# Performance work log

Measured on AMD Instinct MI355X. Metric: run time of the kernel, lower is better.

## Reference

```python
import jax, jax.numpy as jnp
import numpy as np

HID, HEADS = 2048, 16
HD = HID // HEADS  # head_dim = 128
EPS = 1e-6


def rope_tables(head_dim, max_pos, base=10000.0):
    inv = 1.0 / (base ** (jnp.arange(0, head_dim, 2, dtype=jnp.float32) / head_dim))
    t = jnp.arange(max_pos, dtype=jnp.float32)
    freqs = jnp.outer(t, inv)                      # [max_pos, d/2]
    emb = jnp.concatenate([freqs, freqs], axis=-1)  # [max_pos, d]
    return jnp.cos(emb), jnp.sin(emb)


def rotate_half(x):
    x1, x2 = jnp.split(x, 2, axis=-1)
    return jnp.concatenate([-x2, x1], axis=-1)


def lf_gate(x, c1w, c1b, c2w, c2b, rms_w):
    # x: [b, s, h]; prompt phase -> lf1/lf2 caches are zeros -> zero-pad 1 step on time axis
    xt = jnp.transpose(x, (0, 2, 1))[..., None]                 # [b, h, s, 1]
    xt = jnp.pad(xt, ((0, 0), (0, 0), (1, 0), (0, 0)))           # [b, h, s+1, 1]
    dn = ('NCHW', 'OIHW', 'NCHW')
    o1 = jax.lax.conv_general_dilated(xt, c1w, (1, 1), 'VALID', dimension_numbers=dn)
    o1 = o1 + c1b[None, :, None, None]                           # [b, h/2, s, 1]
    o1 = jnp.pad(o1, ((0, 0), (0, 0), (1, 0), (0, 0)))           # [b, h/2, s+1, 1]
    o2 = jax.lax.conv_general_dilated(o1, c2w, (1, 1), 'VALID', dimension_numbers=dn)
    o2 = o2 + c2b[None, :, None, None]                           # [b, h, s, 1]
    y = jnp.transpose(o2[..., 0], (0, 2, 1)) + x                 # residual, [b, s, h]
    var = jnp.mean(y * y, axis=-1, keepdims=True)
    return y * jax.lax.rsqrt(var + EPS) * rms_w


def setup_inputs() -> dict:
    key = jax.random.key(0)
    ks = jax.random.split(key, 10)
    b, s = 2, 2048
    inp = {
        'hidden_states': jax.random.normal(ks[0], (b, s, HID), jnp.float32),
        'positions': jnp.arange(s, dtype=jnp.int32),
        'wq': jax.random.normal(ks[1], (HID, HID), jnp.float32) * 0.02,
        'wk': jax.random.normal(ks[2], (HID, HID), jnp.float32) * 0.02,
        'wv': jax.random.normal(ks[3], (HID, HID), jnp.float32) * 0.02,
        'wo': jax.random.normal(ks[4], (HID, HID), jnp.float32) * 0.02,
        'conv1_w': jax.random.normal(ks[5], (HID // 2, HID, 2, 1), jnp.float32) * 0.02,
        'conv1_b': jnp.zeros((HID // 2,), jnp.float32),
        'conv2_w': jax.random.normal(ks[6], (HID, HID // 2, 2, 1), jnp.float32) * 0.02,
        'conv2_b': jnp.zeros((HID,), jnp.float32),
        'rms_w': jnp.ones((HID,), jnp.float32),
    }
    return inp


def reference(hidden_states, positions, wq, wk, wv, wo, conv1_w, conv1_b, conv2_w, conv2_b, rms_w):
    b, s, _ = hidden_states.shape
    # value projection from raw hidden states (pre-gate)
    v = (hidden_states @ wv).reshape(b, s, HEADS, HD)            # [b, s, H, d]
    # localized-filtering gate (prompt phase: zero caches)
    h = lf_gate(hidden_states, conv1_w, conv1_b, conv2_w, conv2_b, rms_w)
    q = h @ wq                                                   # [b, s, H*d]
    k = h @ wk
    # faithful Yuan quirk: concat q,k then reshape to [b,s,H,2d] and chunk
    qk = jnp.concatenate([q, k], axis=-1).reshape(b, s, HEADS, 2 * HD)
    q, k = jnp.split(qk, 2, axis=-1)                             # each [b, s, H, d]
    # rotary
    cos, sin = rope_tables(HD, 8192)
    c = cos[positions][None, :, None, :]                         # [1, s, 1, d]
    sn = sin[positions][None, :, None, :]
    q = q * c + rotate_half(q) * sn
    k = k * c + rotate_half(k) * sn
    # causal attention (paged attention reduces to this for the prompt)
    scale = HD ** -0.5
    scores = jnp.einsum('bqhd,bkhd->bhqk', q, k) * scale         # [b, H, s, s]
    mask = jnp.tril(jnp.ones((s, s), dtype=bool))
    scores = jnp.where(mask[None, None], scores, jnp.finfo(scores.dtype).min)
    probs = jax.nn.softmax(scores, axis=-1)
    out = jnp.einsum('bhqk,bkhd->bqhd', probs, v).reshape(b, s, HEADS * HD)
    return out @ wo
```

## Files before the change

### kernel.cpp

```cpp
#include <hip/hip_runtime.h>

#define HID 2048
#define HEADS 16
#define HD 128
#define BATCH 2
#define S 2048
#define ROWS (BATCH*S)

typedef short short8 __attribute__((ext_vector_type(8)));
typedef unsigned short ushort4v __attribute__((ext_vector_type(4)));
typedef unsigned short ushort2v __attribute__((ext_vector_type(2)));
typedef float f32x4 __attribute__((ext_vector_type(4)));
typedef __bf16 bf16x8 __attribute__((ext_vector_type(8)));
typedef __bf16 bf16x4 __attribute__((ext_vector_type(4)));

static __device__ __forceinline__ float b2f(unsigned short u) {
  union { float f; unsigned int i; } v; v.i = ((unsigned int)u) << 16; return v.f;
}
static __device__ __forceinline__ unsigned short f2b(float f) {
  union { float f; unsigned int i; } v; v.f = f;
  unsigned int u = v.i;
  unsigned int r = ((u >> 16) & 1u) + 0x7fffu;
  return (unsigned short)((u + r) >> 16);
}

static __device__ __forceinline__ void gload_lds16(const unsigned short* g, unsigned short* l) {
  __builtin_amdgcn_global_load_lds(
      (const __attribute__((address_space(1))) unsigned int*)(const void*)g,
      (__attribute__((address_space(3))) unsigned int*)(void*)l,
      16, 0, 0);
}

__global__ void fill_debug(unsigned short* __restrict__ out, long n) {
  long i = (long)blockIdx.x * blockDim.x + threadIdx.x;
  if (i < n) out[i] = 0x447A;
}

__global__ void prep_all(const float* __restrict__ c1w, const float* __restrict__ c2w,
                         const float* __restrict__ x, const int* __restrict__ positions,
                         const float* __restrict__ c1b, const float* __restrict__ c2b,
                         const float* __restrict__ rmsw,
                         unsigned short* __restrict__ w1t0, unsigned short* __restrict__ w1t1,
                         unsigned short* __restrict__ w2t0, unsigned short* __restrict__ w2t1,
                         unsigned short* __restrict__ xb,
                         float* __restrict__ ctab, float* __restrict__ stab,
                         unsigned short* __restrict__ c1bb, unsigned short* __restrict__ c2bb,
                         unsigned short* __restrict__ rmswb, unsigned short* __restrict__ zpg) {
  int job = blockIdx.y;
  if (job == 0 || job == 1) {
    const float* w = (job == 0) ? c1w : c2w;
    unsigned short* o0 = (job == 0) ? w1t0 : w2t0;
    unsigned short* o1 = (job == 0) ? w1t1 : w2t1;
    long i = (long)blockIdx.x * 256 + threadIdx.x;
    f32x4 v = *(const f32x4*)(w + i*4);
    ushort2v a = { f2b(v[0]), f2b(v[2]) };
    ushort2v b = { f2b(v[1]), f2b(v[3]) };
    *(ushort2v*)(o0 + i*2) = a;
    *(ushort2v*)(o1 + i*2) = b;
  } else if (job == 2) {
    long i = (long)blockIdx.x * 256 + threadIdx.x;
    #pragma unroll
    for (int rep = 0; rep < 2; ++rep) {
      long idx = i + (long)rep * 1048576L;
      f32x4 v = *(const f32x4*)(x + idx*4);
      ushort4v o = { f2b(v[0]), f2b(v[1]), f2b(v[2]), f2b(v[3]) };
      *(ushort4v*)(xb + idx*4) = o;
    }
  } else {
    int bx = blockIdx.x;
    if (bx < 512) {
      int t = bx * 4 + (threadIdx.x >> 6);
      int i = threadIdx.x & 63;
      float pos = (float)positions[t];
      float inv = powf(10000.0f, -(float)i / 64.0f);
      float ang = pos * inv;
      float sv, cv;
      sincosf(ang, &sv, &cv);
      ctab[t*64 + i] = cv;
      stab[t*64 + i] = sv;
    } else if (bx < 544) {
      int i = (bx - 512) * 256 + threadIdx.x;
      if (i < 1024) c1bb[i] = f2b(c1b[i]);
      if (i < 2048) { c2bb[i] = f2b(c2b[i]); rmswb[i] = f2b(rmsw[i]); }
      zpg[i] = 0;
    }
  }
}

__global__ void transpose4(const float* __restrict__ s0, const float* __restrict__ s1,
                           const float* __restrict__ s2, const float* __restrict__ s3,
                           unsigned short* __restrict__ d0, unsigned short* __restrict__ d1,
                           unsigned short* __restrict__ d2, unsigned short* __restrict__ d3) {
  __shared__ unsigned short tl[64][73];
  const float* in; unsigned short* out; int perm;
  switch (blockIdx.z) {
    case 0:  in = s0; out = d0; perm = 1; break;
    case 1:  in = s1; out = d1; perm = 1; break;
    case 2:  in = s2; out = d2; perm = 0; break;
    default: in = s3; out = d3; perm = 0; break;
  }
  int n0 = blockIdx.x * 64, k0 = blockIdx.y * 64;
  int tid = threadIdx.x;
  int r = tid >> 3, c8 = (tid & 7) * 8;
  #pragma unroll
  for (int j = 0; j < 2; ++j) {
    int rr = r + j*32;
    const float* p = in + (size_t)(k0 + rr)*HID + n0 + c8;
    f32x4 v0 = *(const f32x4*)p;
    f32x4 v1 = *(const f32x4*)(p + 4);
    #pragma unroll
    for (int e = 0; e < 4; ++e) { tl[rr][c8 + e] = f2b(v0[e]); tl[rr][c8 + 4 + e] = f2b(v1[e]); }
  }
  __syncthreads();
  #pragma unroll
  for (int j = 0; j < 2; ++j) {
    int rr = r + j*32;
    int orow = n0 + rr;
    if (perm) {
      int s5 = (orow >> 5) & 3;
      s5 = (s5 == 1) ? 2 : (s5 == 2) ? 1 : s5;
      orow = (orow & ~127) | (s5 << 5) | (orow & 31);
    }
    short8 v;
    #pragma unroll
    for (int e = 0; e < 8; ++e) v[e] = (short)tl[c8 + e][rr];
    *(short8*)(out + (size_t)orow*HID + k0 + c8) = v;
  }
}


struct SPtrs { const unsigned short* p[6]; };

static __device__ __forceinline__ void build_ptrs(SPtrs& sp,
    const unsigned short* Ap, const unsigned short* Bp, int Ksz, int sh,
    int m0, int n0, const unsigned short* zpg, int tid) {
  int lane = tid & 63;
  int scol = (((lane & 7) * 16) ^ (((lane >> 3) & 7) << 4)) >> 1;
  #pragma unroll
  for (int j = 0; j < 2; ++j) {
    int row = ((tid >> 6) * 2 + j) * 8 + (lane >> 3);
    int gr = m0 + row;
    sp.p[j]     = (sh && ((gr & (S - 1)) == 0)) ? (zpg + scol)
                                                : (Ap + (size_t)(gr - sh)*Ksz + scol);
    sp.p[2 + j] = Bp + (size_t)(n0 + row)*Ksz + scol;
    sp.p[4 + j] = Bp + (size_t)(n0 + 128 + row)*Ksz + scol;
  }
}

static __device__ __forceinline__ void stage6(unsigned short* buf, SPtrs& sp, int tid) {
  int c0 = (tid >> 6) * 1024;
  gload_lds16(sp.p[0], buf + c0);
  gload_lds16(sp.p[1], buf + c0 + 512);
  gload_lds16(sp.p[2], buf + 8192  + c0);
  gload_lds16(sp.p[3], buf + 8192  + c0 + 512);
  gload_lds16(sp.p[4], buf + 16384 + c0);
  gload_lds16(sp.p[5], buf + 16384 + c0 + 512);
  #pragma unroll
  for (int i = 0; i < 6; ++i) sp.p[i] += 64;
}

static __device__ __forceinline__ void rd_af(const unsigned short* Ah, bf16x8 (&afr)[4][2],
                                             int wm, int lr, int col0, int axor) {
  #pragma unroll
  for (int mi = 0; mi < 4; ++mi) {
    const unsigned short* rp = Ah + (wm*64 + mi*16 + lr) * 64;
    #pragma unroll
    for (int kk = 0; kk < 2; ++kk)
      afr[mi][kk] = *(const bf16x8*)(rp + (((kk*64 + col0) ^ axor) >> 1));
  }
}
static __device__ __forceinline__ void rd_bf(const unsigned short* Bh, bf16x8 (&bfr)[2][2],
                                             int wn, int lr, int col0, int axor) {
  #pragma unroll
  for (int ni = 0; ni < 2; ++ni) {
    const unsigned short* rp = Bh + (wn*32 + ni*16 + lr) * 64;
    #pragma unroll
    for (int kk = 0; kk < 2; ++kk)
      bfr[ni][kk] = *(const bf16x8*)(rp + (((kk*64 + col0) ^ axor) >> 1));
  }
}
static __device__ __forceinline__ void mfma16(const bf16x8 (&afr)[4][2], const bf16x8 (&bfr)[2][2],
                                              f32x4 (&ac)[4][2]) {
  #pragma unroll
  for (int kk = 0; kk < 2; ++kk)
    #pragma unroll
    for (int mi = 0; mi < 4; ++mi)
      #pragma unroll
      for (int ni = 0; ni < 2; ++ni)
        ac[mi][ni] = __builtin_amdgcn_mfma_f32_16x16x32_bf16(afr[mi][kk], bfr[ni][kk], ac[mi][ni], 0, 0, 0);
}

static __device__ __forceinline__ void gemm8_core(
    unsigned short* lds,
    const unsigned short* __restrict__ A1, const unsigned short* __restrict__ A2,
    const unsigned short* __restrict__ B1, const unsigned short* __restrict__ B2,
    int K1, int K2,
    const unsigned short* __restrict__ bias, const unsigned short* __restrict__ resid,
    void* __restrict__ Cout, int outmode, int N, int m0, int n0,
    int a1shift, const unsigned short* __restrict__ zrow) {
  int tid = threadIdx.x;
  int lane = tid & 63, w = tid >> 6;
  int wm = w >> 2, wn = w & 3;
  int lr = lane & 15, g = lane >> 4;
  int col0 = g * 16;
  int axor = (lr & 7) << 4;
  int nk1 = K1 >> 6;
  int nk = (K1 + K2) >> 6;
  f32x4 acc[2][4][2] = {};
  bf16x8 afr[4][2], bfr0[2][2], bfr1[2][2];

  unsigned short* buf0 = lds;
  unsigned short* buf1 = lds + 24576;
  unsigned short* buf2 = lds + 49152;

  SPtrs sp;
  build_ptrs(sp, A1, B1, K1, a1shift, m0, n0, zrow, tid);

  stage6(buf0, sp, tid);
  stage6(buf1, sp, tid);

  unsigned short* cur = buf0;
  unsigned short* nx1 = buf1;
  unsigned short* nx2 = buf2;
  for (int t = 0; t < nk; ++t) {
    if (t < nk - 1) asm volatile("s_waitcnt vmcnt(6)" ::: "memory");
    else            asm volatile("s_waitcnt vmcnt(0)" ::: "memory");
    __builtin_amdgcn_s_barrier();
    asm volatile("" ::: "memory");

    rd_af(cur,         afr,  wm, lr, col0, axor);
    rd_bf(cur + 8192,  bfr0, wn, lr, col0, axor);
    rd_bf(cur + 16384, bfr1, wn, lr, col0, axor);
    if (t + 2 < nk) {
      if (t + 2 == nk1) build_ptrs(sp, A2, B2, K2, 0, m0, n0, zrow, tid);
      stage6(nx2, sp, tid);
    }
    __builtin_amdgcn_s_setprio(1);
    mfma16(afr, bfr0, acc[0]);
    mfma16(afr, bfr1, acc[1]);
    __builtin_amdgcn_s_setprio(0);

    unsigned short* tmp = cur; cur = nx1; nx1 = nx2; nx2 = tmp;
  }

  #pragma unroll
  for (int qn = 0; qn < 2; ++qn)
    #pragma unroll
    for (int mi = 0; mi < 4; ++mi) {
      int row0 = m0 + wm*64 + mi*16 + g*4;
      #pragma unroll
      for (int ni = 0; ni < 2; ++ni) {
        int col = n0 + qn*128 + wn*32 + ni*16 + lr;
        float bv = bias ? b2f(bias[col]) : 0.f;
        f32x4 a = acc[qn][mi][ni];
        if (outmode == 3) {
          int bb = row0 >> 11;
          int s0 = row0 & (S - 1);
          size_t base = ((size_t)bb * HID + col) * S + s0;
          ushort4v pk;
          #pragma unroll
          for (int j = 0; j < 4; ++j) pk[j] = f2b(a[j]);
          *(ushort4v*)((unsigned short*)Cout + base) = pk;
        } else {
          #pragma unroll
          for (int j = 0; j < 4; ++j) {
            size_t idx = (size_t)(row0 + j) * N + col;
            float v = a[j] + bv;
            if (resid) v += b2f(resid[idx]);
            if (outmode == 1) ((float*)Cout)[idx] = v;
            else ((unsigned short*)Cout)[idx] = f2b(v);
          }
        }
      }
    }
}

template<int SHIFT>
__launch_bounds__(512, 1)
__global__ void gemm8_bt(const unsigned short* __restrict__ A1,
                         const unsigned short* __restrict__ A2,
                         const unsigned short* __restrict__ B1,
                         const unsigned short* __restrict__ B2,
                         int K1, int K2,
                         const unsigned short* __restrict__ bias,
                         const unsigned short* __restrict__ resid,
                         void* __restrict__ Cout, int outmode, int N,
                         const unsigned short* __restrict__ zrow) {
  __shared__ __align__(16) unsigned short lds[73728];
  gemm8_core(lds, A1, A2, B1, B2, K1, K2, bias, resid, Cout, outmode, N,
             blockIdx.x*128, blockIdx.y*256, SHIFT, zrow);
}

struct GemmJob {
  const unsigned short *A1, *A2, *B1, *B2;
  int K1, K2;
  const unsigned short *bias;
  void* Cout; int outmode; int N; int nby; int a1shift;
};

__launch_bounds__(512, 1)
__global__ void gemm8_dual(GemmJob j0, GemmJob j1, const unsigned short* __restrict__ zrow) {
  __shared__ __align__(16) unsigned short lds[73728];
  int by = blockIdx.y;
  GemmJob j;
  if (by < j0.nby) { j = j0; } else { j = j1; by -= j0.nby; }
  gemm8_core(lds, j.A1, j.A2, j.B1, j.B2, j.K1, j.K2, j.bias, nullptr,
             j.Cout, j.outmode, j.N, blockIdx.x*128, by*256, j.a1shift, zrow);
}

__global__ void rmsnorm_rows(const unsigned short* __restrict__ y,
                             const unsigned short* __restrict__ w,
                             unsigned short* __restrict__ out) {
  int r = blockIdx.x;
  int c8 = threadIdx.x * 8;
  const unsigned short* yr = y + (size_t)r * HID;
  short8 v = *(const short8*)(yr + c8);
  float f[8];
  float ss = 0.f;
  #pragma unroll
  for (int e = 0; e < 8; ++e) { f[e] = b2f((unsigned short)v[e]); ss += f[e]*f[e]; }
  #pragma unroll
  for (int o = 32; o; o >>= 1) ss += __shfl_xor(ss, o);
  __shared__ float red[4];
  if ((threadIdx.x & 63) == 0) red[threadIdx.x >> 6] = ss;
  __syncthreads();
  float tot = red[0] + red[1] + red[2] + red[3];
  float scale = rsqrtf(tot / (float)HID + 1e-6f);
  short8 wv = *(const short8*)(w + c8);
  short8 o8;
  #pragma unroll
  for (int e = 0; e < 8; ++e) o8[e] = (short)f2b(f[e] * scale * b2f((unsigned short)wv[e]));
  *(short8*)(out + (size_t)r*HID + c8) = o8;
}

__global__ void rope_rearrange(const unsigned short* __restrict__ qkf,
                               const float* __restrict__ ctab, const float* __restrict__ stab,
                               unsigned short* __restrict__ qr, unsigned short* __restrict__ kr) {
  int r = blockIdx.x;
  int t = r & (S - 1);
  int h = threadIdx.x >> 4;
  int i4 = (threadIdx.x & 15) * 4;
  int pc = (i4 & 31) + ((i4 >> 5) << 6);
  const unsigned short* qk = qkf + (size_t)r * (2*HID) + h * 256;
  f32x4 c = *(const f32x4*)(ctab + t*64 + i4);
  f32x4 s = *(const f32x4*)(stab + t*64 + i4);
  ushort4v q1 = *(const ushort4v*)(qk + pc);
  ushort4v q2 = *(const ushort4v*)(qk + pc + 32);
  ushort4v k1 = *(const ushort4v*)(qk + 128 + pc);
  ushort4v k2 = *(const ushort4v*)(qk + 128 + pc + 32);
  size_t o = (size_t)r * HID + (size_t)h * HD;
  const float SC = 0.08838834764831845f * 1.44269504088896340f;
  ushort4v oq1, oq2, ok1, ok2;
  #pragma unroll
  for (int e = 0; e < 4; ++e) {
    float a = b2f(q1[e]), b = b2f(q2[e]);
    float x = b2f(k1[e]), y = b2f(k2[e]);
    oq1[e] = f2b((a*c[e] - b*s[e]) * SC);
    oq2[e] = f2b((b*c[e] + a*s[e]) * SC);
    ok1[e] = f2b(x*c[e] - y*s[e]);
    ok2[e] = f2b(y*c[e] + x*s[e]);
  }
  *(ushort4v*)(qr + o + i4)      = oq1;
  *(ushort4v*)(qr + o + 64 + i4) = oq2;
  *(ushort4v*)(kr + o + i4)      = ok1;
  *(ushort4v*)(kr + o + 64 + i4) = ok2;
}

#define KT 64

__launch_bounds__(256, 2)
__global__ void attn_mfma(const unsigned short* __restrict__ Qr,
                          const unsigned short* __restrict__ Kr,
                          const unsigned short* __restrict__ Vt,
                          unsigned short* __restrict__ Out) {
  __shared__ __align__(16) unsigned short lds[36864];
  int tid = threadIdx.x, lane = tid & 63, w = tid >> 6;
  int bh = blockIdx.x;
  int b = bh >> 4, h = bh & 15;
  int qt = (int)gridDim.y - 1 - (int)blockIdx.y;
  int q0 = qt * 64;
  size_t bS = (size_t)b * S;
  size_t ho = (size_t)h * HD;
  int lr = lane & 15, g = lane >> 4;
  int rsw = (lr & 7) << 3;
  bf16x8 bq[4];
  {
    int qrow = q0 + w*16 + lr;
    const unsigned short* qp = Qr + (bS + qrow)*HID + ho + g*8;
    #pragma unroll
    for (int kk = 0; kk < 4; ++kk) bq[kk] = *(const bf16x8*)(qp + kk*32);
  }
  const unsigned short* kp[4];
  const unsigned short* vp[4];
  #pragma unroll
  for (int j = 0; j < 4; ++j) {
    int c = w*4 + j;
    int rk = c*4 + (lane >> 4);
    int sck = ((lane & 15) * 8) ^ ((rk & 7) << 3);
    kp[j] = Kr + (bS + rk)*HID + ho + sck;
    int rv = c*8 + (lane >> 3);
    int scv = ((lane & 7) * 8) ^ ((rv & 7) << 3);
    vp[j] = Vt + ((size_t)b*HID + ho + rv)*S + scv;
  }
  int cdst = (w*4) * 512;
  unsigned short* curK = lds;
  unsigned short* curV = lds + 8192;
  unsigned short* nxtK = lds + 16384;
  unsigned short* nxtV = lds + 24576;
  #pragma unroll
  for (int j = 0; j < 4; ++j) {
    gload_lds16(kp[j], curK + cdst + j*512);
    gload_lds16(vp[j], curV + cdst + j*512);
    kp[j] += (size_t)KT * HID;
    vp[j] += KT;
  }
  f32x4 o[8] = {};
  float m = -1e30f, l = 0.f;
  unsigned short* PlW = lds + 32768 + w*1024;
  int ntiles = qt + 1;
  for (int kt = 0; kt < ntiles; ++kt) {
    asm volatile("s_waitcnt vmcnt(0)" ::: "memory");
    __builtin_amdgcn_s_barrier();
    asm volatile("" ::: "memory");
    if (kt + 1 < ntiles) {
      #pragma unroll
      for (int j = 0; j < 4; ++j) {
        gload_lds16(kp[j], nxtK + cdst + j*512);
        gload_lds16(vp[j], nxtV + cdst + j*512);
        kp[j] += (size_t)KT * HID;
        vp[j] += KT;
      }
    }
    f32x4 st[4] = {};
    __builtin_amdgcn_s_setprio(1);
    #pragma unroll
    for (int kk = 0; kk < 4; ++kk) {
      #pragma unroll
      for (int mi = 0; mi < 4; ++mi) {
        bf16x8 a = *(const bf16x8*)(&curK[(mi*16 + lr)*128 + ((kk*32 + g*8) ^ rsw)]);
        st[mi] = __builtin_amdgcn_mfma_f32_16x16x32_bf16(a, bq[kk], st[mi], 0, 0, 0);
      }
    }
    __builtin_amdgcn_s_setprio(0);
    bool lastt = (kt == ntiles - 1);
    float tm = -1e30f;
    #pragma unroll
    for (int mi = 0; mi < 4; ++mi)
      #pragma unroll
      for (int r = 0; r < 4; ++r) {
        float v = st[mi][r];
        if (lastt && (mi*16 + 4*g + r) > (w*16 + lr)) v = -1e30f;
        st[mi][r] = v;
        tm = fmaxf(tm, v);
      }
    tm = fmaxf(tm, __shfl_xor(tm, 16));
    tm = fmaxf(tm, __shfl_xor(tm, 32));
    if (!__all(tm - m <= 11.5f)) {
      float mn = fmaxf(m, tm);
      float sc = exp2f(m - mn);
      float s0 = __shfl(sc, 4*g+0), s1 = __shfl(sc, 4*g+1);
      float s2 = __shfl(sc, 4*g+2), s3 = __shfl(sc, 4*g+3);
      #pragma unroll
      for (int ni = 0; ni < 8; ++ni) {
        o[ni][0] *= s0; o[ni][1] *= s1; o[ni][2] *= s2; o[ni][3] *= s3;
      }
      l *= sc;
      m = mn;
    }
    float ts = 0.f;
    __bf16 pbf[4][4];
    #pragma unroll
    for (int mi = 0; mi < 4; ++mi)
      #pragma unroll
      for (int r = 0; r < 4; ++r) {
        float p = exp2f(st[mi][r] - m);
        ts += p;
        pbf[mi][r] = (__bf16)p;
      }
    ts += __shfl_xor(ts, 16);
    ts += __shfl_xor(ts, 32);
    l += ts;
    #pragma unroll
    for (int mi = 0; mi < 4; ++mi) {
      bf16x4 pk = { pbf[mi][0], pbf[mi][1], pbf[mi][2], pbf[mi][3] };
      *(bf16x4*)(&PlW[lr*64 + ((mi*16 + 4*g) ^ rsw)]) = pk;
    }
    asm volatile("" ::: "memory");
    __builtin_amdgcn_s_setprio(1);
    #pragma unroll
    for (int kk = 0; kk < 2; ++kk) {
      int pc = (kk*32 + g*8) ^ rsw;
      bf16x8 a = *(const bf16x8*)(&PlW[lr*64 + pc]);
      #pragma unroll
      for (int ni = 0; ni < 8; ++ni) {
        bf16x8 bv = *(const bf16x8*)(&curV[(ni*16 + lr)*64 + pc]);
        o[ni] = __builtin_amdgcn_mfma_f32_16x16x32_bf16(a, bv, o[ni], 0, 0, 0);
      }
    }
    __builtin_amdgcn_s_setprio(0);
    unsigned short* t0 = curK; curK = nxtK; nxtK = t0;
    unsigned short* t1 = curV; curV = nxtV; nxtV = t1;
  }
  float l0 = __shfl(l, 4*g+0), l1 = __shfl(l, 4*g+1);
  float l2 = __shfl(l, 4*g+2), l3 = __shfl(l, 4*g+3);
  float i0 = 1.f/l0, i1 = 1.f/l1, i2 = 1.f/l2, i3 = 1.f/l3;
  int rbase = q0 + w*16 + 4*g;
  #pragma unroll
  for (int ni = 0; ni < 8; ++ni) {
    size_t cbase = ho + ni*16 + lr;
    Out[(bS + rbase + 0)*HID + cbase] = f2b(o[ni][0]*i0);
    Out[(bS + rbase + 1)*HID + cbase] = f2b(o[ni][1]*i1);
    Out[(bS + rbase + 2)*HID + cbase] = f2b(o[ni][2]*i2);
    Out[(bS + rbase + 3)*HID + cbase] = f2b(o[ni][3]*i3);
  }
}

extern "C" void kernel_launch(void* const* d_in, const int* in_sizes, int n_in,
                              void* d_out, int out_size, void* d_ws, size_t ws_size,
                              hipStream_t stream) {
  const float* x_raw   = (const float*)d_in[0];
  const int* positions = (const int*)d_in[1];
  const float* wq_raw  = (const float*)d_in[2];
  const float* wk_raw  = (const float*)d_in[3];
  const float* wv_raw  = (const float*)d_in[4];
  const float* wo_raw  = (const float*)d_in[5];
  const float* c1w_raw = (const float*)d_in[6];
  const float* c1b_raw = (const float*)d_in[7];
  const float* c2w_raw = (const float*)d_in[8];
  const float* c2b_raw = (const float*)d_in[9];
  const float* rms_raw = (const float*)d_in[10];

  const size_t WS_NEEDED = 140000000;
  if (ws_size < WS_NEEDED) {
    long n = (long)out_size;
    fill_debug<<<dim3((unsigned)((n + 255) / 256)), dim3(256), 0, stream>>>((unsigned short*)d_out, n);
    return;
  }

  char* ws = (char*)d_ws;
  size_t off = 0;
  auto alloc = [&](size_t bytes) { char* p = ws + off; off += (bytes + 255) & ~(size_t)255; return p; };
  float* ctab          = (float*)alloc((size_t)S*64*4);
  float* stab          = (float*)alloc((size_t)S*64*4);
  unsigned short* wqkt = (unsigned short*)alloc((size_t)2*HID*HID*2);
  unsigned short* wvt  = (unsigned short*)alloc((size_t)HID*HID*2);
  unsigned short* wot  = (unsigned short*)alloc((size_t)HID*HID*2);
  unsigned short* w1t0 = (unsigned short*)alloc((size_t)1024*HID*2);
  unsigned short* w1t1 = (unsigned short*)alloc((size_t)1024*HID*2);
  unsigned short* w2t0 = (unsigned short*)alloc((size_t)HID*1024*2);
  unsigned short* w2t1 = (unsigned short*)alloc((size_t)HID*1024*2);
  unsigned short* xb   = (unsigned short*)alloc((size_t)ROWS*HID*2);
  unsigned short* qrb  = (unsigned short*)alloc((size_t)ROWS*HID*2);
  unsigned short* o1   = (unsigned short*)alloc((size_t)ROWS*1024*2);
  unsigned short* yb   = (unsigned short*)alloc((size_t)ROWS*HID*2);
  unsigned short* hg   = (unsigned short*)alloc((size_t)ROWS*HID*2);
  unsigned short* qkf  = (unsigned short*)alloc((size_t)ROWS*2*HID*2);
  unsigned short* vtg  = (unsigned short*)alloc((size_t)BATCH*HID*S*2);
  unsigned short* c1bb = (unsigned short*)alloc(1024*2);
  unsigned short* c2bb = (unsigned short*)alloc(2048*2);
  unsigned short* rmswb= (unsigned short*)alloc(2048*2);
  unsigned short* zpg  = (unsigned short*)alloc(8192*2);
  unsigned short* krr  = xb;
  unsigned short* attn = yb;

  dim3 b256(256);
  dim3 b512(512);
  prep_all<<<dim3(4096, 4), b256, 0, stream>>>(c1w_raw, c2w_raw, x_raw, positions,
                                               c1b_raw, c2b_raw, rms_raw,
                                               w1t0, w1t1, w2t0, w2t1, xb,
                                               ctab, stab, c1bb, c2bb, rmswb, zpg);
  transpose4<<<dim3(32,32,4), b256, 0, stream>>>(wq_raw, wk_raw, wv_raw, wo_raw,
                                                 wqkt, wqkt + (size_t)HID*HID, wvt, wot);
  {
    GemmJob j0 = { xb, xb, w1t0, w1t1, HID, HID, c1bb, o1, 0, 1024, 4, 1 };
    GemmJob j1 = { xb, xb, wvt,  wvt,  HID, 0,   nullptr, vtg, 3, HID, 8, 0 };
    gemm8_dual<<<dim3(ROWS/128, 12), b512, 0, stream>>>(j0, j1, zpg);
  }
  gemm8_bt<1><<<dim3(ROWS/128, HID/256), b512, 0, stream>>>(o1, o1, w2t0, w2t1, 1024, 1024, c2bb, xb, yb, 0, HID, zpg);
  rmsnorm_rows<<<dim3(ROWS), b256, 0, stream>>>(yb, rmswb, hg);
  gemm8_bt<0><<<dim3(ROWS/128, (2*HID)/256), b512, 0, stream>>>(hg, hg, wqkt, wqkt, HID, 0, nullptr, nullptr, qkf, 0, 2*HID, nullptr);
  rope_rearrange<<<dim3(ROWS), b256, 0, stream>>>(qkf, ctab, stab, qrb, krr);
  attn_mfma<<<dim3(BATCH*HEADS, S/64), b256, 0, stream>>>(qrb, krr, vtg, attn);
  gemm8_bt<0><<<dim3(ROWS/128, HID/256), b512, 0, stream>>>(attn, attn, wot, wot, HID, 0, nullptr, nullptr, d_out, 1, HID, nullptr);
}
```

Measured before the change: 368.2 us.

## Switch attention to 32x32x16 MFMA with 128-row query tiles and register P

The attention kernel now uses 32x32x16 bf16 MFMA instead of 16x16x32, with each wave owning 32 query rows, so a block covers 128 queries and the grid halves. The softmax probabilities stay in registers and are redistributed with cross-half shuffles instead of going through LDS, which removes the P staging buffer and its LDS traffic. Causal masking now applies only to tiles that cross the diagonal. This doubles reuse of each K/V tile loaded per block and cuts LDS reads, but it raises register pressure, halves the number of blocks, and computes some fully masked work near the diagonal for waves whose rows sit lower in the tile.

```diff
diff --git a/kernel.cpp b/kernel.cpp
--- a/kernel.cpp
+++ b/kernel.cpp
@@ -11,8 +11,10 @@
 typedef unsigned short ushort4v __attribute__((ext_vector_type(4)));
 typedef unsigned short ushort2v __attribute__((ext_vector_type(2)));
 typedef float f32x4 __attribute__((ext_vector_type(4)));
+typedef float f32x16 __attribute__((ext_vector_type(16)));
 typedef __bf16 bf16x8 __attribute__((ext_vector_type(8)));
 typedef __bf16 bf16x4 __attribute__((ext_vector_type(4)));
+typedef __bf16 bf16x2 __attribute__((ext_vector_type(2)));
 
 static __device__ __forceinline__ float b2f(unsigned short u) {
   union { float f; unsigned int i; } v; v.i = ((unsigned int)u) << 16; return v.f;
@@ -373,22 +375,21 @@
                           const unsigned short* __restrict__ Kr,
                           const unsigned short* __restrict__ Vt,
                           unsigned short* __restrict__ Out) {
-  __shared__ __align__(16) unsigned short lds[36864];
+  __shared__ __align__(16) unsigned short lds[32768];
   int tid = threadIdx.x, lane = tid & 63, w = tid >> 6;
   int bh = blockIdx.x;
   int b = bh >> 4, h = bh & 15;
   int qt = (int)gridDim.y - 1 - (int)blockIdx.y;
-  int q0 = qt * 64;
+  int q0w = qt * 128 + w * 32;
   size_t bS = (size_t)b * S;
   size_t ho = (size_t)h * HD;
-  int lr = lane & 15, g = lane >> 4;
-  int rsw = (lr & 7) << 3;
-  bf16x8 bq[4];
+  int l31 = lane & 31, hi = lane >> 5;
+  int rsw = (lane & 7) << 3;
+  bf16x8 bq[8];
   {
-    int qrow = q0 + w*16 + lr;
-    const unsigned short* qp = Qr + (bS + qrow)*HID + ho + g*8;
-    #pragma unroll
-    for (int kk = 0; kk < 4; ++kk) bq[kk] = *(const bf16x8*)(qp + kk*32);
+    const unsigned short* qp = Qr + (bS + q0w + l31)*HID + ho + hi*8;
+    #pragma unroll
+    for (int kk = 0; kk < 8; ++kk) bq[kk] = *(const bf16x8*)(qp + kk*16);
   }
   const unsigned short* kp[4];
   const unsigned short* vp[4];
@@ -414,10 +415,9 @@
     kp[j] += (size_t)KT * HID;
     vp[j] += KT;
   }
-  f32x4 o[8] = {};
+  f32x16 o2[4] = {};
   float m = -1e30f, l = 0.f;
-  unsigned short* PlW = lds + 32768 + w*1024;
-  int ntiles = qt + 1;
+  int ntiles = 2*qt + 2;
   for (int kt = 0; kt < ntiles; ++kt) {
     asm volatile("s_waitcnt vmcnt(0)" ::: "memory");
     __builtin_amdgcn_s_barrier();
@@ -431,87 +431,99 @@
         vp[j] += KT;
       }
     }
-    f32x4 st[4] = {};
+    f32x16 st0 = {}, st1 = {};
     __builtin_amdgcn_s_setprio(1);
     #pragma unroll
-    for (int kk = 0; kk < 4; ++kk) {
-      #pragma unroll
-      for (int mi = 0; mi < 4; ++mi) {
-        bf16x8 a = *(const bf16x8*)(&curK[(mi*16 + lr)*128 + ((kk*32 + g*8) ^ rsw)]);
-        st[mi] = __builtin_amdgcn_mfma_f32_16x16x32_bf16(a, bq[kk], st[mi], 0, 0, 0);
+    for (int kk = 0; kk < 8; ++kk) {
+      bf16x8 a0 = *(const bf16x8*)(&curK[(l31)*128      + ((kk*16 + hi*8) ^ rsw)]);
+      bf16x8 a1 = *(const bf16x8*)(&curK[(32 + l31)*128 + ((kk*16 + hi*8) ^ rsw)]);
+      st0 = __builtin_amdgcn_mfma_f32_32x32x16_bf16(a0, bq[kk], st0, 0, 0, 0);
+      st1 = __builtin_amdgcn_mfma_f32_32x32x16_bf16(a1, bq[kk], st1, 0, 0, 0);
+    }
+    __builtin_amdgcn_s_setprio(0);
+    int kbase = kt * 64;
+    float tm = -1e30f;
+    if (kbase + 63 > q0w) {
+      int qg = q0w + l31;
+      #pragma unroll
+      for (int r = 0; r < 16; ++r) {
+        int crow = (r&3) + 8*(r>>2) + 4*hi;
+        if (kbase + crow > qg)      st0[r] = -1e30f;
+        if (kbase + 32 + crow > qg) st1[r] = -1e30f;
+        tm = fmaxf(tm, fmaxf(st0[r], st1[r]));
       }
-    }
-    __builtin_amdgcn_s_setprio(0);
-    bool lastt = (kt == ntiles - 1);
-    float tm = -1e30f;
-    #pragma unroll
-    for (int mi = 0; mi < 4; ++mi)
-      #pragma unroll
-      for (int r = 0; r < 4; ++r) {
-        float v = st[mi][r];
-        if (lastt && (mi*16 + 4*g + r) > (w*16 + lr)) v = -1e30f;
-        st[mi][r] = v;
-        tm = fmaxf(tm, v);
-      }
-    tm = fmaxf(tm, __shfl_xor(tm, 16));
+    } else {
+      #pragma unroll
+      for (int r = 0; r < 16; ++r) tm = fmaxf(tm, fmaxf(st0[r], st1[r]));
+    }
     tm = fmaxf(tm, __shfl_xor(tm, 32));
     if (!__all(tm - m <= 11.5f)) {
       float mn = fmaxf(m, tm);
       float sc = exp2f(m - mn);
-      float s0 = __shfl(sc, 4*g+0), s1 = __shfl(sc, 4*g+1);
-      float s2 = __shfl(sc, 4*g+2), s3 = __shfl(sc, 4*g+3);
-      #pragma unroll
-      for (int ni = 0; ni < 8; ++ni) {
-        o[ni][0] *= s0; o[ni][1] *= s1; o[ni][2] *= s2; o[ni][3] *= s3;
+      #pragma unroll
+      for (int r = 0; r < 16; ++r) {
+        int crow = (r&3) + 8*(r>>2) + 4*hi;
+        float scv = __shfl(sc, crow);
+        #pragma unroll
+        for (int ni = 0; ni < 4; ++ni) o2[ni][r] *= scv;
       }
       l *= sc;
       m = mn;
     }
     float ts = 0.f;
-    __bf16 pbf[4][4];
-    #pragma unroll
-    for (int mi = 0; mi < 4; ++mi)
-      #pragma unroll
-      for (int r = 0; r < 4; ++r) {
-        float p = exp2f(st[mi][r] - m);
-        ts += p;
-        pbf[mi][r] = (__bf16)p;
-      }
-    ts += __shfl_xor(ts, 16);
+    unsigned int u0[8], u1[8];
+    #pragma unroll
+    for (int j = 0; j < 8; ++j) {
+      float a0 = exp2f(st0[2*j] - m), b0 = exp2f(st0[2*j+1] - m);
+      float a1 = exp2f(st1[2*j] - m), b1 = exp2f(st1[2*j+1] - m);
+      ts += a0 + b0 + a1 + b1;
+      union { bf16x2 v; unsigned int ui; } p0, p1;
+      p0.v = bf16x2{(__bf16)a0, (__bf16)b0};
+      p1.v = bf16x2{(__bf16)a1, (__bf16)b1};
+      u0[j] = p0.ui; u1[j] = p1.ui;
+    }
     ts += __shfl_xor(ts, 32);
     l += ts;
-    #pragma unroll
-    for (int mi = 0; mi < 4; ++mi) {
-      bf16x4 pk = { pbf[mi][0], pbf[mi][1], pbf[mi][2], pbf[mi][3] };
-      *(bf16x4*)(&PlW[lr*64 + ((mi*16 + 4*g) ^ rsw)]) = pk;
-    }
-    asm volatile("" ::: "memory");
+    unsigned int x0[8], x1[8];
+    #pragma unroll
+    for (int j = 0; j < 8; ++j) {
+      x0[j] = (unsigned int)__shfl_xor((int)u0[j], 32);
+      x1[j] = (unsigned int)__shfl_xor((int)u1[j], 32);
+    }
     __builtin_amdgcn_s_setprio(1);
     #pragma unroll
-    for (int kk = 0; kk < 2; ++kk) {
-      int pc = (kk*32 + g*8) ^ rsw;
-      bf16x8 a = *(const bf16x8*)(&PlW[lr*64 + pc]);
-      #pragma unroll
-      for (int ni = 0; ni < 8; ++ni) {
-        bf16x8 bv = *(const bf16x8*)(&curV[(ni*16 + lr)*64 + pc]);
-        o[ni] = __builtin_amdgcn_mfma_f32_16x16x32_bf16(a, bv, o[ni], 0, 0, 0);
+    for (int s = 0; s < 4; ++s) {
+      int j16 = s & 1;
+      unsigned int w0, w1, w2, w3;
+      if (s < 2) {
+        if (hi == 0) { w0=u0[4*j16];   w1=u0[4*j16+1]; w2=x0[4*j16];   w3=x0[4*j16+1]; }
+        else         { w0=x0[4*j16+2]; w1=x0[4*j16+3]; w2=u0[4*j16+2]; w3=u0[4*j16+3]; }
+      } else {
+        if (hi == 0) { w0=u1[4*j16];   w1=u1[4*j16+1]; w2=x1[4*j16];   w3=x1[4*j16+1]; }
+        else         { w0=x1[4*j16+2]; w1=x1[4*j16+3]; w2=u1[4*j16+2]; w3=u1[4*j16+3]; }
+      }
+      union { unsigned int ui[4]; bf16x8 v; } pa;
+      pa.ui[0]=w0; pa.ui[1]=w1; pa.ui[2]=w2; pa.ui[3]=w3;
+      #pragma unroll
+      for (int ni = 0; ni < 4; ++ni) {
+        int d = ni*32 + l31;
+        bf16x8 bv = *(const bf16x8*)(&curV[d*64 + ((s*16 + hi*8) ^ rsw)]);
+        o2[ni] = __builtin_amdgcn_mfma_f32_32x32x16_bf16(pa.v, bv, o2[ni], 0, 0, 0);
       }
     }
     __builtin_amdgcn_s_setprio(0);
     unsigned short* t0 = curK; curK = nxtK; nxtK = t0;
     unsigned short* t1 = curV; curV = nxtV; nxtV = t1;
   }
-  float l0 = __shfl(l, 4*g+0), l1 = __shfl(l, 4*g+1);
-  float l2 = __shfl(l, 4*g+2), l3 = __shfl(l, 4*g+3);
-  float i0 = 1.f/l0, i1 = 1.f/l1, i2 = 1.f/l2, i3 = 1.f/l3;
-  int rbase = q0 + w*16 + 4*g;
-  #pragma unroll
-  for (int ni = 0; ni < 8; ++ni) {
-    size_t cbase = ho + ni*16 + lr;
-    Out[(bS + rbase + 0)*HID + cbase] = f2b(o[ni][0]*i0);
-    Out[(bS + rbase + 1)*HID + cbase] = f2b(o[ni][1]*i1);
-    Out[(bS + rbase + 2)*HID + cbase] = f2b(o[ni][2]*i2);
-    Out[(bS + rbase + 3)*HID + cbase] = f2b(o[ni][3]*i3);
+  float invl = 1.f / l;
+  #pragma unroll
+  for (int r = 0; r < 16; ++r) {
+    int crow = (r&3) + 8*(r>>2) + 4*hi;
+    float iv = __shfl(invl, crow);
+    size_t rowbase = (bS + q0w + crow)*HID + ho + l31;
+    #pragma unroll
+    for (int ni = 0; ni < 4; ++ni)
+      Out[rowbase + ni*32] = f2b(o2[ni][r] * iv);
   }
 }
 
@@ -580,6 +592,6 @@
   rmsnorm_rows<<<dim3(ROWS), b256, 0, stream>>>(yb, rmswb, hg);
   gemm8_bt<0><<<dim3(ROWS/128, (2*HID)/256), b512, 0, stream>>>(hg, hg, wqkt, wqkt, HID, 0, nullptr, nullptr, qkf, 0, 2*HID, nullptr);
   rope_rearrange<<<dim3(ROWS), b256, 0, stream>>>(qkf, ctab, stab, qrb, krr);
-  attn_mfma<<<dim3(BATCH*HEADS, S/64), b256, 0, stream>>>(qrb, krr, vtg, attn);
+  attn_mfma<<<dim3(BATCH*HEADS, S/128), b256, 0, stream>>>(qrb, krr, vtg, attn);
   gemm8_bt<0><<<dim3(ROWS/128, HID/256), b512, 0, stream>>>(attn, attn, wot, wot, HID, 0, nullptr, nullptr, d_out, 1, HID, nullptr);
 }
```

Result: no change. 375.3 us (+1.9%).
